# Performance work log

Hardware: AMD Instinct MI355X
Metric: run time of the kernel (lower is better)

The kernel has to match this reference:

```python
import jax, jax.numpy as jnp
import numpy as np

B, T, E = 8, 2048, 2048

def setup_inputs() -> dict:
    key = jax.random.key(0)
    k1, k2, k3 = jax.random.split(key, 3)
    x = jax.random.normal(k1, (B, T, E), dtype=jnp.float32)
    weight = jax.random.normal(k2, (T,), dtype=jnp.float32)
    bias = jax.random.normal(k3, (T,), dtype=jnp.float32)
    return {"x": x, "weight": weight, "bias": bias}

def _toeplitz_matrix(v, T):
    # M[i, j] = v[j - i] for j >= i, else 0  (upper-triangular Toeplitz)
    idx = jnp.arange(T)
    diff = idx[None, :] - idx[:, None]          # [T, T], diff = j - i
    M = jnp.where(diff >= 0, v[jnp.clip(diff, 0, T - 1)], jnp.zeros((), v.dtype))
    return M

def reference(x, weight, bias):
    Tlen = x.shape[1]
    W = _toeplitz_matrix(weight[:Tlen], Tlen).astype(x.dtype)  # [T, T]
    # original: out[b,e,t'] = sum_t x[b,e,t] * W[t,t']; in (B,T,E) layout:
    out = jnp.einsum('bte,ts->bse', x, W)
    out = out + bias[:Tlen][None, :, None]
    return out
```

## Files before the change

### kernel.cpp

```cpp
#include <hip/hip_runtime.h>
#include <hip/hip_bf16.h>

#define T_LEN 2048
#define E_LEN 2048
#define B_SZ  8
#define BM 256
#define BN 256
#define BK2 64
#define WREV_LEN 4104
#define CL 2312
#define ABUF_B 32768
#define BOFF (3 * ABUF_B)

typedef short short8 __attribute__((ext_vector_type(8)));
typedef float floatx4 __attribute__((ext_vector_type(4)));

typedef const __attribute__((address_space(1))) void* gas_ptr;
typedef __attribute__((address_space(3))) void* lds_ptr;

__global__ __launch_bounds__(256) void transpose_cast(
    const float* __restrict__ x, __hip_bfloat16* __restrict__ xT)
{
    const int t0 = blockIdx.x * 64, e0 = blockIdx.y * 64, b = blockIdx.z;
    __shared__ unsigned int W[64][33];
    const int tid = threadIdx.x;
    const int wave = tid >> 6, lane = tid & 63;

    const float* xb = x + (size_t)b * T_LEN * E_LEN;
    const int c = tid & 15;
    const int q = tid >> 4;

    #pragma unroll
    for (int i = 0; i < 2; ++i) {
        const int tp = q + 16 * i;
        const float4 a4 = *reinterpret_cast<const float4*>(
            xb + (size_t)(t0 + 2 * tp) * E_LEN + e0 + 4 * c);
        const float4 b4 = *reinterpret_cast<const float4*>(
            xb + (size_t)(t0 + 2 * tp + 1) * E_LEN + e0 + 4 * c);
        const float av[4] = {a4.x, a4.y, a4.z, a4.w};
        const float bv[4] = {b4.x, b4.y, b4.z, b4.w};
        #pragma unroll
        for (int j = 0; j < 4; ++j) {
            __hip_bfloat16 ha = __float2bfloat16(av[j]);
            __hip_bfloat16 hb = __float2bfloat16(bv[j]);
            unsigned int w =
                (unsigned int)*reinterpret_cast<unsigned short*>(&ha) |
                ((unsigned int)*reinterpret_cast<unsigned short*>(&hb) << 16);
            W[4 * c + j][tp] = w;
        }
    }
    __syncthreads();

    __hip_bfloat16* xTb = xT + (size_t)b * E_LEN * T_LEN;
    const int er = lane >> 3;
    const int pc = (lane & 7) * 4;
    #pragma unroll
    for (int i = 0; i < 2; ++i) {
        const int e = wave * 8 + i * 32 + er;
        uint4 v;
        v.x = W[e][pc + 0];
        v.y = W[e][pc + 1];
        v.z = W[e][pc + 2];
        v.w = W[e][pc + 3];
        unsigned int* dst =
            reinterpret_cast<unsigned int*>(xTb + (size_t)(e0 + e) * T_LEN + t0);
        *reinterpret_cast<uint4*>(dst + pc) = v;
    }
}

__global__ __launch_bounds__(256) void build_wrevs(
    const float* __restrict__ w, __hip_bfloat16* __restrict__ wrevs)
{
    int total = 8 * WREV_LEN;
    for (int i = threadIdx.x + blockIdx.x * blockDim.x; i < total;
         i += blockDim.x * gridDim.x) {
        int p = i / WREV_LEN, q = i - p * WREV_LEN;
        int j = q + p;
        float v = (j < T_LEN) ? w[T_LEN - 1 - j] : 0.0f;
        wrevs[i] = __float2bfloat16(v);
    }
}

#define LOAD_A(MH)                                                             \
    _Pragma("unroll")                                                          \
    for (int m4 = 0; m4 < 4; ++m4) {                                           \
        const int r = arow + ((MH) * 4 + m4) * 16;                             \
        afr[m4][0] = *reinterpret_cast<const short8*>(Ab + r * 128 + xq0 * 16);\
        afr[m4][1] = *reinterpret_cast<const short8*>(Ab + r * 128 + xq1 * 16);\
    }

#define LOAD_B(NH)                                                             \
    _Pragma("unroll")                                                          \
    for (int n2 = 0; n2 < 2; ++n2) {                                           \
        _Pragma("unroll")                                                      \
        for (int kk = 0; kk < 2; ++kk) {                                       \
            const int C = Cb + t0 + kk * 32 - ((NH) * 2 + n2) * 16;            \
            const int p = C & 7;                                               \
            bfr[n2][kk] = *reinterpret_cast<const short8*>(                    \
                L + BOFF + p * (CL * 2) + ((C - p) - Wbase) * 2);              \
        }                                                                      \
    }

#define MFMA16(MH, NH)                                                         \
    _Pragma("unroll")                                                          \
    for (int kk = 0; kk < 2; ++kk)                                             \
        _Pragma("unroll")                                                      \
        for (int m4 = 0; m4 < 4; ++m4)                                         \
            _Pragma("unroll")                                                  \
            for (int n2 = 0; n2 < 2; ++n2)                                     \
                acc[(MH) * 4 + m4][(NH) * 2 + n2] =                            \
                    __builtin_amdgcn_mfma_f32_16x16x32_bf16(                   \
                        afr[m4][kk], bfr[n2][kk],                              \
                        acc[(MH) * 4 + m4][(NH) * 2 + n2], 0, 0, 0);

#define PHASE_SYNC_PRE()                                                       \
    __builtin_amdgcn_s_barrier();                                              \
    asm volatile("s_waitcnt lgkmcnt(0)" ::: "memory");                         \
    __builtin_amdgcn_sched_barrier(0);                                         \
    __builtin_amdgcn_s_setprio(1);

#define PHASE_SYNC_POST()                                                      \
    __builtin_amdgcn_s_setprio(0);                                             \
    __builtin_amdgcn_s_barrier();

__global__ __launch_bounds__(512, 2) void toeplitz_gemm(
    const __hip_bfloat16* __restrict__ xT,
    const __hip_bfloat16* __restrict__ wrevs,
    const float* __restrict__ bias,
    float* __restrict__ out)
{
    __shared__ __align__(16) char L[3 * ABUF_B + 8 * CL * 2];

    const int bid = blockIdx.x;
    const int lid = (bid & 7) * 64 + (bid >> 3);
    const int nb = 7 - (lid & 7);
    const int panel = lid >> 3;
    const int mb = panel & 7, b = panel >> 3;
    const int e0 = mb * BM, s0 = nb * BN;
    const int tid = threadIdx.x;
    const int wave = tid >> 6, lane = tid & 63;
    const int wm = (wave >> 2) * 128;
    const int wn = (wave & 3) * 64;
    const int ln15 = lane & 15, quad = lane >> 4, ln7 = lane & 7;

    const int ktiles = (s0 + BN) / BK2;
    const int Wbase = T_LEN - 264 - s0;
    const __hip_bfloat16* xTb = xT + ((size_t)b * E_LEN + e0) * T_LEN;

    for (int i = tid; i < 8 * (CL / 8); i += 512) {
        const int p = i / (CL / 8), c = i - p * (CL / 8);
        int q = Wbase + c * 8;
        if (q < 0) q = 0;
        const uint4 v = *(reinterpret_cast<const uint4*>(
            wrevs + (size_t)p * WREV_LEN + q));
        *(reinterpret_cast<uint4*>(L + BOFF + (size_t)p * (CL * 2)) + c) = v;
    }
    __syncthreads();

    floatx4 acc[8][4];
    #pragma unroll
    for (int i = 0; i < 8; ++i)
        #pragma unroll
        for (int j = 0; j < 4; ++j)
            acc[i][j] = (floatx4){0.f, 0.f, 0.f, 0.f};

    auto STAGE1 = [&](int buf, int kt2, int cc) {
        const int t0n = kt2 * BK2;
        const int c = cc * 512 + tid;
        const int r = c >> 3, p = c & 7;
        const int ps = p ^ (r & 7);
        const __hip_bfloat16* g = xTb + (size_t)r * T_LEN + t0n + ps * 8;
        __builtin_amdgcn_global_load_lds(
            (gas_ptr)g,
            (lds_ptr)(L + buf * ABUF_B + (cc * 512 + wave * 64) * 16), 16, 0, 0);
    };

    STAGE1(0, 0, 0); STAGE1(0, 0, 1); STAGE1(0, 0, 2); STAGE1(0, 0, 3);
    STAGE1(1, 1, 0); STAGE1(1, 1, 1); STAGE1(1, 1, 2); STAGE1(1, 1, 3);
    asm volatile("s_waitcnt vmcnt(4)" ::: "memory");
    __builtin_amdgcn_s_barrier();

    const int arow = wm + ln15;
    const int xq0 = quad ^ ln7;
    const int xq1 = (4 + quad) ^ ln7;
    const int Cb = (T_LEN - 1 - s0 - wn - ln15) + quad * 8;

    short8 afr[4][2], bfr[2][2];
    int bi = 0;
    for (int kt = 0; kt < ktiles; ++kt) {
        const int t0 = kt * BK2;
        const char* Ab = L + bi * ABUF_B;
        const int pf = (kt + 2 < ktiles);
        const int bp = (bi + 2 >= 3) ? bi - 1 : bi + 2;

        LOAD_A(0) LOAD_B(0)
        if (pf) STAGE1(bp, kt + 2, 0);
        PHASE_SYNC_PRE()
        MFMA16(0, 0)
        PHASE_SYNC_POST()

        LOAD_A(1)
        if (pf) STAGE1(bp, kt + 2, 1);
        PHASE_SYNC_PRE()
        MFMA16(1, 0)
        PHASE_SYNC_POST()

        LOAD_B(1)
        if (pf) STAGE1(bp, kt + 2, 2);
        PHASE_SYNC_PRE()
        MFMA16(1, 1)
        PHASE_SYNC_POST()

        LOAD_A(0)
        if (pf) STAGE1(bp, kt + 2, 3);
        PHASE_SYNC_PRE()
        MFMA16(0, 1)
        __builtin_amdgcn_s_setprio(0);
        if (pf) asm volatile("s_waitcnt vmcnt(4)" ::: "memory");
        else    asm volatile("s_waitcnt vmcnt(0)" ::: "memory");
        __builtin_amdgcn_s_barrier();

        bi = (bi + 1 == 3) ? 0 : bi + 1;
    }

    #pragma unroll
    for (int ni = 0; ni < 4; ++ni) {
        const int s = s0 + wn + ni * 16 + ln15;
        const float bv = bias[s];
        #pragma unroll
        for (int mi = 0; mi < 8; ++mi) {
            const int e = e0 + wm + mi * 16 + quad * 4;
            float* dst = out + ((size_t)b * T_LEN + s) * E_LEN + e;
            floatx4 v = acc[mi][ni];
            v.x += bv; v.y += bv; v.z += bv; v.w += bv;
            *reinterpret_cast<floatx4*>(dst) = v;
        }
    }
}

extern "C" void kernel_launch(void* const* d_in, const int* in_sizes, int n_in,
                              void* d_out, int out_size, void* d_ws, size_t ws_size,
                              hipStream_t stream)
{
    const float* x    = (const float*)d_in[0];
    const float* w    = (const float*)d_in[1];
    const float* bias = (const float*)d_in[2];
    float* out = (float*)d_out;

    __hip_bfloat16* xT = (__hip_bfloat16*)d_ws;
    __hip_bfloat16* wrevs =
        (__hip_bfloat16*)((char*)d_ws + (size_t)B_SZ * E_LEN * T_LEN * 2);

    transpose_cast<<<dim3(T_LEN / 64, E_LEN / 64, B_SZ), 256, 0, stream>>>(x, xT);
    build_wrevs<<<dim3(64), 256, 0, stream>>>(w, wrevs);
    toeplitz_gemm<<<dim3(512), 512, 0, stream>>>(xT, wrevs, bias, out);
}
```

Before: 346.4 us.

## Pair triangular tiles per block for load balance and simplify MFMA pipeline

Halves the grid to 256 blocks and has each block process two column tiles (nb = 7-pi and pi), so every block does the same total number of k-tiles across the triangular Toeplitz workload. The per-k-tile loop is also restructured: all four prefetch stages are issued up front, A/B fragments for both k halves are loaded, and MFMAs are done in two 32-instruction groups without the intermediate barriers of the four-phase schedule. This targets tail imbalance from uneven triangular work and barrier overhead, at the cost of fewer concurrent blocks and possibly less LDS/MFMA interleaving and higher register pressure.

```diff
diff --git a/kernel.cpp b/kernel.cpp
--- a/kernel.cpp
+++ b/kernel.cpp
@@ -81,47 +81,30 @@
     }
 }
 
-#define LOAD_A(MH)                                                             \
+#define LOAD_A8(dst, KK)                                                       \
     _Pragma("unroll")                                                          \
-    for (int m4 = 0; m4 < 4; ++m4) {                                           \
-        const int r = arow + ((MH) * 4 + m4) * 16;                             \
-        afr[m4][0] = *reinterpret_cast<const short8*>(Ab + r * 128 + xq0 * 16);\
-        afr[m4][1] = *reinterpret_cast<const short8*>(Ab + r * 128 + xq1 * 16);\
-    }
-
-#define LOAD_B(NH)                                                             \
+    for (int mi = 0; mi < 8; ++mi) {                                           \
+        const int r = wm + mi * 16 + ln15;                                     \
+        const int xq = ((KK) * 4 + quad) ^ (ln15 & 7);                         \
+        dst[mi] = *reinterpret_cast<const short8*>(Ab + r * 128 + xq * 16);    \
+    }
+
+#define LOAD_B4(dst, KK)                                                       \
     _Pragma("unroll")                                                          \
-    for (int n2 = 0; n2 < 2; ++n2) {                                           \
+    for (int ni = 0; ni < 4; ++ni) {                                           \
+        const int C = Cb + t0 + (KK) * 32 - ni * 16;                           \
+        const int p = C & 7;                                                   \
+        dst[ni] = *reinterpret_cast<const short8*>(                            \
+            L + BOFF + p * (CL * 2) + ((C - p) - Wbase) * 2);                  \
+    }
+
+#define MFMA32(Af, Bf)                                                         \
+    _Pragma("unroll")                                                          \
+    for (int ni = 0; ni < 4; ++ni)                                             \
         _Pragma("unroll")                                                      \
-        for (int kk = 0; kk < 2; ++kk) {                                       \
-            const int C = Cb + t0 + kk * 32 - ((NH) * 2 + n2) * 16;            \
-            const int p = C & 7;                                               \
-            bfr[n2][kk] = *reinterpret_cast<const short8*>(                    \
-                L + BOFF + p * (CL * 2) + ((C - p) - Wbase) * 2);              \
-        }                                                                      \
-    }
-
-#define MFMA16(MH, NH)                                                         \
-    _Pragma("unroll")                                                          \
-    for (int kk = 0; kk < 2; ++kk)                                             \
-        _Pragma("unroll")                                                      \
-        for (int m4 = 0; m4 < 4; ++m4)                                         \
-            _Pragma("unroll")                                                  \
-            for (int n2 = 0; n2 < 2; ++n2)                                     \
-                acc[(MH) * 4 + m4][(NH) * 2 + n2] =                            \
-                    __builtin_amdgcn_mfma_f32_16x16x32_bf16(                   \
-                        afr[m4][kk], bfr[n2][kk],                              \
-                        acc[(MH) * 4 + m4][(NH) * 2 + n2], 0, 0, 0);
-
-#define PHASE_SYNC_PRE()                                                       \
-    __builtin_amdgcn_s_barrier();                                              \
-    asm volatile("s_waitcnt lgkmcnt(0)" ::: "memory");                         \
-    __builtin_amdgcn_sched_barrier(0);                                         \
-    __builtin_amdgcn_s_setprio(1);
-
-#define PHASE_SYNC_POST()                                                      \
-    __builtin_amdgcn_s_setprio(0);                                             \
-    __builtin_amdgcn_s_barrier();
+        for (int mi = 0; mi < 8; ++mi)                                         \
+            acc[mi][ni] = __builtin_amdgcn_mfma_f32_16x16x32_bf16(             \
+                Af[mi], Bf[ni], acc[mi][ni], 0, 0, 0);
 
 __global__ __launch_bounds__(512, 2) void toeplitz_gemm(
     const __hip_bfloat16* __restrict__ xT,
@@ -132,108 +115,105 @@
     __shared__ __align__(16) char L[3 * ABUF_B + 8 * CL * 2];
 
     const int bid = blockIdx.x;
-    const int lid = (bid & 7) * 64 + (bid >> 3);
-    const int nb = 7 - (lid & 7);
-    const int panel = lid >> 3;
+    const int xcd = bid & 7, r5 = bid >> 3;
+    const int panel = xcd * 8 + (r5 & 7);
+    const int pi = r5 >> 3;
     const int mb = panel & 7, b = panel >> 3;
-    const int e0 = mb * BM, s0 = nb * BN;
+    const int e0 = mb * BM;
     const int tid = threadIdx.x;
     const int wave = tid >> 6, lane = tid & 63;
     const int wm = (wave >> 2) * 128;
     const int wn = (wave & 3) * 64;
-    const int ln15 = lane & 15, quad = lane >> 4, ln7 = lane & 7;
-
-    const int ktiles = (s0 + BN) / BK2;
-    const int Wbase = T_LEN - 264 - s0;
+    const int ln15 = lane & 15, quad = lane >> 4;
+
     const __hip_bfloat16* xTb = xT + ((size_t)b * E_LEN + e0) * T_LEN;
-
-    for (int i = tid; i < 8 * (CL / 8); i += 512) {
-        const int p = i / (CL / 8), c = i - p * (CL / 8);
-        int q = Wbase + c * 8;
-        if (q < 0) q = 0;
-        const uint4 v = *(reinterpret_cast<const uint4*>(
-            wrevs + (size_t)p * WREV_LEN + q));
-        *(reinterpret_cast<uint4*>(L + BOFF + (size_t)p * (CL * 2)) + c) = v;
-    }
-    __syncthreads();
-
-    floatx4 acc[8][4];
-    #pragma unroll
-    for (int i = 0; i < 8; ++i)
-        #pragma unroll
-        for (int j = 0; j < 4; ++j)
-            acc[i][j] = (floatx4){0.f, 0.f, 0.f, 0.f};
 
     auto STAGE1 = [&](int buf, int kt2, int cc) {
         const int t0n = kt2 * BK2;
         const int c = cc * 512 + tid;
-        const int r = c >> 3, p = c & 7;
-        const int ps = p ^ (r & 7);
-        const __hip_bfloat16* g = xTb + (size_t)r * T_LEN + t0n + ps * 8;
+        const int rr = c >> 3, p = c & 7;
+        const int ps = p ^ (rr & 7);
+        const __hip_bfloat16* g = xTb + (size_t)rr * T_LEN + t0n + ps * 8;
         __builtin_amdgcn_global_load_lds(
             (gas_ptr)g,
             (lds_ptr)(L + buf * ABUF_B + (cc * 512 + wave * 64) * 16), 16, 0, 0);
     };
 
-    STAGE1(0, 0, 0); STAGE1(0, 0, 1); STAGE1(0, 0, 2); STAGE1(0, 0, 3);
-    STAGE1(1, 1, 0); STAGE1(1, 1, 1); STAGE1(1, 1, 2); STAGE1(1, 1, 3);
-    asm volatile("s_waitcnt vmcnt(4)" ::: "memory");
-    __builtin_amdgcn_s_barrier();
-
-    const int arow = wm + ln15;
-    const int xq0 = quad ^ ln7;
-    const int xq1 = (4 + quad) ^ ln7;
-    const int Cb = (T_LEN - 1 - s0 - wn - ln15) + quad * 8;
-
-    short8 afr[4][2], bfr[2][2];
-    int bi = 0;
-    for (int kt = 0; kt < ktiles; ++kt) {
-        const int t0 = kt * BK2;
-        const char* Ab = L + bi * ABUF_B;
-        const int pf = (kt + 2 < ktiles);
-        const int bp = (bi + 2 >= 3) ? bi - 1 : bi + 2;
-
-        LOAD_A(0) LOAD_B(0)
-        if (pf) STAGE1(bp, kt + 2, 0);
-        PHASE_SYNC_PRE()
-        MFMA16(0, 0)
-        PHASE_SYNC_POST()
-
-        LOAD_A(1)
-        if (pf) STAGE1(bp, kt + 2, 1);
-        PHASE_SYNC_PRE()
-        MFMA16(1, 0)
-        PHASE_SYNC_POST()
-
-        LOAD_B(1)
-        if (pf) STAGE1(bp, kt + 2, 2);
-        PHASE_SYNC_PRE()
-        MFMA16(1, 1)
-        PHASE_SYNC_POST()
-
-        LOAD_A(0)
-        if (pf) STAGE1(bp, kt + 2, 3);
-        PHASE_SYNC_PRE()
-        MFMA16(0, 1)
-        __builtin_amdgcn_s_setprio(0);
-        if (pf) asm volatile("s_waitcnt vmcnt(4)" ::: "memory");
-        else    asm volatile("s_waitcnt vmcnt(0)" ::: "memory");
+    for (int run = 0; run < 2; ++run) {
+        const int nb = (run == 0) ? 7 - pi : pi;
+        const int s0 = nb * BN;
+        const int ktiles = 4 * (nb + 1);
+        const int Wbase = T_LEN - 264 - s0;
+        const int Cb = (T_LEN - 1 - s0 - wn - ln15) + quad * 8;
+
+        __syncthreads();
+        for (int i = tid; i < 8 * (CL / 8); i += 512) {
+            const int p = i / (CL / 8), c = i - p * (CL / 8);
+            int q = Wbase + c * 8;
+            if (q < 0) q = 0;
+            const uint4 v = *(reinterpret_cast<const uint4*>(
+                wrevs + (size_t)p * WREV_LEN + q));
+            *(reinterpret_cast<uint4*>(L + BOFF + (size_t)p * (CL * 2)) + c) = v;
+        }
+
+        floatx4 acc[8][4];
+        #pragma unroll
+        for (int i = 0; i < 8; ++i)
+            #pragma unroll
+            for (int j = 0; j < 4; ++j)
+                acc[i][j] = (floatx4){0.f, 0.f, 0.f, 0.f};
+
+        STAGE1(0, 0, 0); STAGE1(0, 0, 1); STAGE1(0, 0, 2); STAGE1(0, 0, 3);
+        STAGE1(1, 1, 0); STAGE1(1, 1, 1); STAGE1(1, 1, 2); STAGE1(1, 1, 3);
+        asm volatile("s_waitcnt vmcnt(4) lgkmcnt(0)" ::: "memory");
         __builtin_amdgcn_s_barrier();
 
-        bi = (bi + 1 == 3) ? 0 : bi + 1;
-    }
-
-    #pragma unroll
-    for (int ni = 0; ni < 4; ++ni) {
-        const int s = s0 + wn + ni * 16 + ln15;
-        const float bv = bias[s];
+        int bi = 0;
+        for (int kt = 0; kt < ktiles; ++kt) {
+            const int t0 = kt * BK2;
+            const char* Ab = L + bi * ABUF_B;
+            const bool pf = (kt + 2 < ktiles);
+            const int bp = (bi + 2 >= 3) ? bi - 1 : bi + 2;
+
+            if (pf) {
+                STAGE1(bp, kt + 2, 0); STAGE1(bp, kt + 2, 1);
+                STAGE1(bp, kt + 2, 2); STAGE1(bp, kt + 2, 3);
+            }
+
+            short8 afr0[8], bfr0[4], afr1[8], bfr1[4];
+            LOAD_A8(afr0, 0)
+            LOAD_B4(bfr0, 0)
+            LOAD_A8(afr1, 1)
+
+            __builtin_amdgcn_s_setprio(1);
+            MFMA32(afr0, bfr0)
+            __builtin_amdgcn_s_setprio(0);
+
+            LOAD_B4(bfr1, 1)
+
+            __builtin_amdgcn_s_setprio(1);
+            MFMA32(afr1, bfr1)
+            __builtin_amdgcn_s_setprio(0);
+
+            if (pf) asm volatile("s_waitcnt vmcnt(4)" ::: "memory");
+            else    asm volatile("s_waitcnt vmcnt(0)" ::: "memory");
+            __builtin_amdgcn_s_barrier();
+
+            bi = (bi + 1 == 3) ? 0 : bi + 1;
+        }
+
         #pragma unroll
-        for (int mi = 0; mi < 8; ++mi) {
-            const int e = e0 + wm + mi * 16 + quad * 4;
-            float* dst = out + ((size_t)b * T_LEN + s) * E_LEN + e;
-            floatx4 v = acc[mi][ni];
-            v.x += bv; v.y += bv; v.z += bv; v.w += bv;
-            *reinterpret_cast<floatx4*>(dst) = v;
+        for (int ni = 0; ni < 4; ++ni) {
+            const int s = s0 + wn + ni * 16 + ln15;
+            const float bv = bias[s];
+            #pragma unroll
+            for (int mi = 0; mi < 8; ++mi) {
+                const int e = e0 + wm + mi * 16 + quad * 4;
+                float* dst = out + ((size_t)b * T_LEN + s) * E_LEN + e;
+                floatx4 v = acc[mi][ni];
+                v.x += bv; v.y += bv; v.z += bv; v.w += bv;
+                *reinterpret_cast<floatx4*>(dst) = v;
+            }
         }
     }
 }
@@ -253,5 +233,5 @@
 
     transpose_cast<<<dim3(T_LEN / 64, E_LEN / 64, B_SZ), 256, 0, stream>>>(x, xT);
     build_wrevs<<<dim3(64), 256, 0, stream>>>(w, wrevs);
-    toeplitz_gemm<<<dim3(512), 512, 0, stream>>>(xT, wrevs, bias, out);
-}
+    toeplitz_gemm<<<dim3(256), 512, 0, stream>>>(xT, wrevs, bias, out);
+}
```

Result: faster. 298.9 us (-13.7%).
